# Kernel tuning notes

Hardware: AMD Instinct MI355X
Metric: run time of the kernel (lower is better)

The kernel has to match this reference:

```python
import jax, jax.numpy as jnp
import numpy as np

B, L, H, NH = 32, 512, 256, 4
DH = H // NH
EPS = 1e-12


def setup_inputs() -> dict:
    key = jax.random.key(0)
    ks = jax.random.split(key, 24)
    p = lambda k, shape: 0.02 * jax.random.normal(k, shape, dtype=jnp.float32)
    return {
        "input_tensor": jax.random.normal(ks[0], (B, L, H), dtype=jnp.float32),
        # sorted positive timestamps (seconds-like scale)
        "time_seq": jnp.sort(jax.random.uniform(ks[1], (B, L), dtype=jnp.float32) * 100.0, axis=-1),
        "attention_mask": jnp.zeros((B, 1, L, L), dtype=jnp.float32),
        "item_seq_len": jnp.clip(jax.random.randint(ks[2], (B,), 0, L), 2, L),
        "Wq": p(ks[3], (H, H)), "bq": jnp.zeros((H,), jnp.float32),
        "Wk": p(ks[4], (H, H)), "bk": jnp.zeros((H,), jnp.float32),
        "Wv": p(ks[5], (H, H)), "bv": jnp.zeros((H,), jnp.float32),
        "Wd": p(ks[6], (H, H)), "bd": jnp.zeros((H,), jnp.float32),
        "ln_g": jnp.ones((H,), jnp.float32), "ln_b": jnp.zeros((H,), jnp.float32),
        "Wtq": p(ks[7], (H, H)), "btq": jnp.zeros((H,), jnp.float32),
        "tw1": p(ks[8], (L, L)), "tb1": p(ks[9], (L, L)),
        "tow1": p(ks[10], (L, L)), "tow2": p(ks[11], (L, L)), "tob": p(ks[12], (L, L)),
        "Wt": p(ks[13], (1, 2 * H)), "bt": jnp.zeros((1,), jnp.float32),
    }


def reference(input_tensor, time_seq, attention_mask, item_seq_len,
              Wq, bq, Wk, bk, Wv, bv, Wd, bd, ln_g, ln_b,
              Wtq, btq, tw1, tb1, tow1, tow2, tob, Wt, bt):
    x = input_tensor  # (B, L, H)

    def heads(t):  # (B,L,H) -> (B,NH,L,DH)
        return t.reshape(B, L, NH, DH).transpose(0, 2, 1, 3)

    q = heads(x @ Wq.T + bq)
    k = heads(x @ Wk.T + bk)
    v = heads(x @ Wv.T + bv)

    scores = jnp.einsum('bhqd,bhkd->bhqk', q, k)  # (B,NH,L,L)

    # --- time decay gate ---
    tq = x @ Wtq.T + btq                                  # (B,L,H)
    time_query_key = jnp.tanh(jnp.einsum('bqh,bkh->bqk', tq, x))  # (B,L,L)
    diff = jnp.abs(time_seq[:, :, None] - time_seq[:, None, :])   # |t_i - t_j|
    decay = jnp.tanh(jnp.log1p(diff) * tw1 + tb1)
    decay_gate = tow1 * decay + tow2 * time_query_key + tob       # (B,L,L)
    time_attn = jax.nn.sigmoid(decay_gate)[:, None, :, :]         # (B,1,L,L)

    scores = scores * time_attn / jnp.sqrt(jnp.float32(DH)) + attention_mask
    probs = jax.nn.softmax(scores, axis=-1)

    ctx = jnp.einsum('bhqk,bhkd->bhqd', probs, v)
    ctx = ctx.transpose(0, 2, 1, 3).reshape(B, L, H)

    hs = ctx @ Wd.T + bd + x
    mu = jnp.mean(hs, axis=-1, keepdims=True)
    var = jnp.var(hs, axis=-1, keepdims=True)
    hs = (hs - mu) / jnp.sqrt(var + EPS) * ln_g + ln_b   # (B,L,H)

    bidx = jnp.arange(B)
    emb1 = hs[bidx, item_seq_len - 1]  # (B,H)
    emb2 = hs[bidx, item_seq_len - 2]  # (B,H)
    pred_intervals = jnp.concatenate([emb1, emb2], axis=1) @ Wt.T + bt  # (B,1)
    return hs, pred_intervals
```

## Files before the change

kernel.cpp:

```cpp
#include <hip/hip_runtime.h>
#include <math.h>

#define Bn 32
#define Ln 512
#define Hn 256
#define NHn 4
#define DHn 64

typedef __attribute__((ext_vector_type(8))) short bf16x8;
typedef __attribute__((ext_vector_type(4))) float f32x4;
typedef unsigned int uint32;

__device__ __forceinline__ short f2b(float f) {
    union { float f; uint32 u; } v; v.f = f;
    uint32 r = (v.u + 0x7FFFu + ((v.u >> 16) & 1u)) >> 16;
    return (short)r;
}
__device__ __forceinline__ float b2f(short h) {
    union { uint32 u; float f; } v; v.u = ((uint32)(unsigned short)h) << 16;
    return v.f;
}
__device__ __forceinline__ float fast_tanh(float x) {
    float e = __expf(2.f * x);
    return 1.f - 2.f * __builtin_amdgcn_rcpf(e + 1.f);
}
__device__ __forceinline__ float fast_sigmoid(float x) {
    return __builtin_amdgcn_rcpf(1.f + __expf(-x));
}

__global__ __launch_bounds__(256) void conv_kernel(
    const float* __restrict__ x,
    const float* __restrict__ Wq, const float* __restrict__ Wk,
    const float* __restrict__ Wv, const float* __restrict__ Wtq,
    const float* __restrict__ Wd,
    short* __restrict__ xb, short* __restrict__ wb)
{
    const size_t NLH = (size_t)Bn * Ln * Hn;
    size_t i4 = ((size_t)blockIdx.x * 256 + threadIdx.x) * 4;
    if (i4 < NLH) {
        float4 v = *(const float4*)(x + i4);
        short4 o; o.x = f2b(v.x); o.y = f2b(v.y); o.z = f2b(v.z); o.w = f2b(v.w);
        *(short4*)(xb + i4) = o;
    } else {
        size_t off = i4 - NLH;
        int w = (int)(off >> 16);
        size_t wi = off & 65535;
        const float* src = (w == 0) ? Wq : (w == 1) ? Wk : (w == 2) ? Wv : (w == 3) ? Wtq : Wd;
        float4 v = *(const float4*)(src + wi);
        short4 o; o.x = f2b(v.x); o.y = f2b(v.y); o.z = f2b(v.z); o.w = f2b(v.w);
        *(short4*)(wb + off) = o;
    }
}

struct Acc { f32x4 t[4]; };

__device__ __forceinline__ void gemm_tile_64(
    const short* __restrict__ A,
    const short* __restrict__ Bm,
    int K, short* As, short* Bs, Acc& acc)
{
    const int tid = threadIdx.x;
    const int lane = tid & 63, w = tid >> 6;
    const int quad = lane >> 4, lm = lane & 15;
    const int srow = tid >> 3;
    const int slot = tid & 7;

    for (int k0 = 0; k0 < K; k0 += 64) {
        __syncthreads();
#pragma unroll
        for (int iss = 0; iss < 2; ++iss) {
            int r = srow + iss * 32;
            bf16x8 av = *(const bf16x8*)(A + (size_t)r * K + k0 + slot * 8);
            bf16x8 bv = *(const bf16x8*)(Bm + (size_t)r * K + k0 + slot * 8);
            *(bf16x8*)(As + r * 72 + slot * 8) = av;
            *(bf16x8*)(Bs + r * 72 + slot * 8) = bv;
        }
        __syncthreads();
#pragma unroll
        for (int ks = 0; ks < 2; ++ks) {
            bf16x8 a = *(const bf16x8*)(As + (w * 16 + lm) * 72 + ks * 32 + quad * 8);
#pragma unroll
            for (int kt = 0; kt < 4; ++kt) {
                bf16x8 b = *(const bf16x8*)(Bs + (kt * 16 + lm) * 72 + ks * 32 + quad * 8);
                acc.t[kt] = __builtin_amdgcn_mfma_f32_16x16x32_bf16(a, b, acc.t[kt], 0, 0, 0);
            }
        }
    }
}

__global__ __launch_bounds__(256) void proj_kernel(
    const short* __restrict__ xb, const short* __restrict__ wb,
    const float* __restrict__ bq, const float* __restrict__ bk,
    const float* __restrict__ bv, const float* __restrict__ btq,
    short* __restrict__ qb, short* __restrict__ kb,
    short* __restrict__ vt, short* __restrict__ tqb)
{
    __shared__ short As[64 * 72];
    __shared__ short Bs[64 * 72];
    const int tensor = blockIdx.x >> 2;
    const int ncol0 = (blockIdx.x & 3) * 64;
    const int m0 = blockIdx.y * 64;
    const short* A = xb + (size_t)m0 * Hn;
    const short* Bw = wb + (size_t)tensor * 65536 + (size_t)ncol0 * Hn;
    const float* bias = (tensor == 0) ? bq : (tensor == 1) ? bk : (tensor == 2) ? bv : btq;

    Acc acc;
#pragma unroll
    for (int i = 0; i < 4; ++i) acc.t[i] = (f32x4){0.f, 0.f, 0.f, 0.f};
    gemm_tile_64(A, Bw, Hn, As, Bs, acc);

    const int lane = threadIdx.x & 63, w = threadIdx.x >> 6;
    const int quad = lane >> 4, lm = lane & 15;

    if (tensor == 2) {
#pragma unroll
        for (int kt = 0; kt < 4; ++kt) {
            int n = ncol0 + kt * 16 + lm;
            float bs = bv[n];
            int h = n >> 6, d = n & 63;
#pragma unroll
            for (int r = 0; r < 4; ++r) {
                int row = m0 + w * 16 + quad * 4 + r;
                int bb = row >> 9, l = row & 511;
                vt[((size_t)(bb * NHn + h) * DHn + d) * Ln + l] = f2b(acc.t[kt][r] + bs);
            }
        }
    } else {
        short* out = (tensor == 0) ? qb : (tensor == 1) ? kb : tqb;
#pragma unroll
        for (int kt = 0; kt < 4; ++kt) {
            int n = ncol0 + kt * 16 + lm;
            float bs = bias[n];
#pragma unroll
            for (int r = 0; r < 4; ++r) {
                int row = m0 + w * 16 + quad * 4 + r;
                out[(size_t)row * Hn + n] = f2b(acc.t[kt][r] + bs);
            }
        }
    }
}

__global__ __launch_bounds__(256) void gate_kernel(
    const short* __restrict__ tqb, const short* __restrict__ xb,
    const float* __restrict__ tseq,
    const float* __restrict__ tw1, const float* __restrict__ tb1,
    const float* __restrict__ tow1, const float* __restrict__ tow2,
    const float* __restrict__ tob,
    short* __restrict__ gateb)
{
    __shared__ short As[64 * 72];
    __shared__ short Bs[64 * 72];
    const int b = blockIdx.z;
    const int m0 = blockIdx.y * 64, n0 = blockIdx.x * 64;
    const short* A = tqb + ((size_t)b * Ln + m0) * Hn;
    const short* Bw = xb + ((size_t)b * Ln + n0) * Hn;

    Acc acc;
#pragma unroll
    for (int i = 0; i < 4; ++i) acc.t[i] = (f32x4){0.f, 0.f, 0.f, 0.f};
    gemm_tile_64(A, Bw, Hn, As, Bs, acc);

    const int lane = threadIdx.x & 63, w = threadIdx.x >> 6;
    const int quad = lane >> 4, lm = lane & 15;
    const float* ts = tseq + (size_t)b * Ln;
    short* go = gateb + (size_t)b * Ln * Ln;
    float ti[4];
#pragma unroll
    for (int r = 0; r < 4; ++r) ti[r] = ts[m0 + w * 16 + quad * 4 + r];
#pragma unroll
    for (int kt = 0; kt < 4; ++kt) {
        int j = n0 + kt * 16 + lm;
        float tj = ts[j];
#pragma unroll
        for (int r = 0; r < 4; ++r) {
            int i = m0 + w * 16 + quad * 4 + r;
            size_t ij = (size_t)i * Ln + j;
            float lg = __logf(1.f + fabsf(ti[r] - tj));
            float dec = fast_tanh(lg * tw1[ij] + tb1[ij]);
            float tqk = fast_tanh(acc.t[kt][r]);
            float dg = tow1[ij] * dec + tow2[ij] * tqk + tob[ij];
            float g = 0.125f * fast_sigmoid(dg);
            go[ij] = f2b(g);
        }
    }
}

__global__ __launch_bounds__(256) void flash_mfma(
    const short* __restrict__ qb, const short* __restrict__ kb,
    const short* __restrict__ vt, const short* __restrict__ gateb,
    const float* __restrict__ mask, short* __restrict__ ctxb)
{
    __shared__ short Ks[64 * 72];
    __shared__ short Vt[64 * 72];
    __shared__ short Ps[4 * 16 * 72];
    const int h = blockIdx.x;
    const int q0 = blockIdx.y * 64;
    const int b = blockIdx.z;
    const int tid = threadIdx.x;
    const int w = tid >> 6, lane = tid & 63;
    const int quad = lane >> 4, lm = lane & 15;
    const int srow = tid >> 3, slot = tid & 7;

    bf16x8 qf0, qf1;
    {
        const short* qrow = qb + ((size_t)(b * Ln + q0 + w * 16 + lm)) * Hn + h * DHn;
        qf0 = *(const bf16x8*)(qrow + quad * 8);
        qf1 = *(const bf16x8*)(qrow + 32 + quad * 8);
    }

    f32x4 o[4];
#pragma unroll
    for (int i = 0; i < 4; ++i) o[i] = (f32x4){0.f, 0.f, 0.f, 0.f};
    float m_run[4] = {-INFINITY, -INFINITY, -INFINITY, -INFINITY};
    float l_run[4] = {0.f, 0.f, 0.f, 0.f};
    const short* gr_base = gateb + (size_t)b * Ln * Ln;
    const float* mk_base = mask + (size_t)b * Ln * Ln;
    const int qrow0 = q0 + w * 16 + quad * 4;
    const short* kbase = kb + ((size_t)(b * Ln)) * Hn + h * DHn;
    const short* vbase = vt + (size_t)(b * NHn + h) * DHn * Ln;

    for (int k0 = 0; k0 < Ln; k0 += 64) {
        __syncthreads();
#pragma unroll
        for (int iss = 0; iss < 2; ++iss) {
            int r = srow + iss * 32;
            bf16x8 kv = *(const bf16x8*)(kbase + (size_t)(k0 + r) * Hn + slot * 8);
            bf16x8 vv = *(const bf16x8*)(vbase + (size_t)r * Ln + k0 + slot * 8);
            *(bf16x8*)(Ks + r * 72 + slot * 8) = kv;
            *(bf16x8*)(Vt + r * 72 + slot * 8) = vv;
        }
        __syncthreads();

        f32x4 s[4];
#pragma unroll
        for (int kt = 0; kt < 4; ++kt) {
            s[kt] = (f32x4){0.f, 0.f, 0.f, 0.f};
            bf16x8 b0 = *(const bf16x8*)(Ks + (kt * 16 + lm) * 72 + quad * 8);
            s[kt] = __builtin_amdgcn_mfma_f32_16x16x32_bf16(qf0, b0, s[kt], 0, 0, 0);
            bf16x8 b1 = *(const bf16x8*)(Ks + (kt * 16 + lm) * 72 + 32 + quad * 8);
            s[kt] = __builtin_amdgcn_mfma_f32_16x16x32_bf16(qf1, b1, s[kt], 0, 0, 0);
        }

        float mnew[4];
#pragma unroll
        for (int r = 0; r < 4; ++r) mnew[r] = m_run[r];
#pragma unroll
        for (int kt = 0; kt < 4; ++kt) {
            int col = k0 + kt * 16 + lm;
#pragma unroll
            for (int r = 0; r < 4; ++r) {
                float g  = b2f(gr_base[(size_t)(qrow0 + r) * Ln + col]);
                float mv = mk_base[(size_t)(qrow0 + r) * Ln + col];
                float sv = s[kt][r] * g + mv;
                s[kt][r] = sv;
                mnew[r] = fmaxf(mnew[r], sv);
            }
        }
        float alpha[4], rsum[4];
#pragma unroll
        for (int r = 0; r < 4; ++r) {
#pragma unroll
            for (int off = 1; off < 16; off <<= 1)
                mnew[r] = fmaxf(mnew[r], __shfl_xor(mnew[r], off, 64));
            alpha[r] = __expf(m_run[r] - mnew[r]);
            m_run[r] = mnew[r];
            rsum[r] = 0.f;
        }
        float p[4][4];
#pragma unroll
        for (int kt = 0; kt < 4; ++kt)
#pragma unroll
            for (int r = 0; r < 4; ++r) {
                float pv = __expf(s[kt][r] - m_run[r]);
                p[kt][r] = pv;
                rsum[r] += pv;
            }
#pragma unroll
        for (int r = 0; r < 4; ++r) {
#pragma unroll
            for (int off = 1; off < 16; off <<= 1) rsum[r] += __shfl_xor(rsum[r], off, 64);
            l_run[r] = l_run[r] * alpha[r] + rsum[r];
#pragma unroll
            for (int ot = 0; ot < 4; ++ot) o[ot][r] *= alpha[r];
        }
        short* pw = Ps + w * 16 * 72;
#pragma unroll
        for (int kt = 0; kt < 4; ++kt)
#pragma unroll
            for (int r = 0; r < 4; ++r)
                pw[(quad * 4 + r) * 72 + kt * 16 + lm] = f2b(p[kt][r]);

#pragma unroll
        for (int ks = 0; ks < 2; ++ks) {
            bf16x8 pa = *(const bf16x8*)(pw + lm * 72 + ks * 32 + quad * 8);
#pragma unroll
            for (int ot = 0; ot < 4; ++ot) {
                bf16x8 vv = *(const bf16x8*)(Vt + (ot * 16 + lm) * 72 + ks * 32 + quad * 8);
                o[ot] = __builtin_amdgcn_mfma_f32_16x16x32_bf16(pa, vv, o[ot], 0, 0, 0);
            }
        }
    }

    float inv[4];
#pragma unroll
    for (int r = 0; r < 4; ++r) inv[r] = 1.0f / l_run[r];
#pragma unroll
    for (int ot = 0; ot < 4; ++ot) {
        int d = h * DHn + ot * 16 + lm;
#pragma unroll
        for (int r = 0; r < 4; ++r) {
            int row = b * Ln + qrow0 + r;
            ctxb[(size_t)row * Hn + d] = f2b(o[ot][r] * inv[r]);
        }
    }
}

__global__ __launch_bounds__(256) void outproj_ln_kernel(
    const short* __restrict__ ctxb, const short* __restrict__ wdb,
    const float* __restrict__ bd, const float* __restrict__ x,
    const float* __restrict__ g, const float* __restrict__ beta,
    float* __restrict__ out)
{
    const int m0 = blockIdx.x * 64;
    const int tid = threadIdx.x;
    const int lane = tid & 63, w = tid >> 6;
    const int quad = lane >> 4, lm = lane & 15;

    const short* arow = ctxb + (size_t)(m0 + w * 16 + lm) * Hn;
    bf16x8 af[8];
#pragma unroll
    for (int k8 = 0; k8 < 8; ++k8)
        af[k8] = *(const bf16x8*)(arow + k8 * 32 + quad * 8);

    f32x4 acc[4][4];
#pragma unroll
    for (int i = 0; i < 4; ++i)
#pragma unroll
        for (int j = 0; j < 4; ++j) acc[i][j] = (f32x4){0.f, 0.f, 0.f, 0.f};

#pragma unroll
    for (int k8 = 0; k8 < 8; ++k8) {
#pragma unroll
        for (int nt = 0; nt < 4; ++nt)
#pragma unroll
            for (int kt = 0; kt < 4; ++kt) {
                bf16x8 bf = *(const bf16x8*)(wdb + (size_t)(nt * 64 + kt * 16 + lm) * Hn + k8 * 32 + quad * 8);
                acc[nt][kt] = __builtin_amdgcn_mfma_f32_16x16x32_bf16(af[k8], bf, acc[nt][kt], 0, 0, 0);
            }
    }

    const int rl0 = w * 16 + quad * 4;
    float s1[4] = {0.f, 0.f, 0.f, 0.f}, s2[4] = {0.f, 0.f, 0.f, 0.f};
#pragma unroll
    for (int nt = 0; nt < 4; ++nt)
#pragma unroll
        for (int kt = 0; kt < 4; ++kt) {
            int col = nt * 64 + kt * 16 + lm;
            float bdv = bd[col];
#pragma unroll
            for (int r = 0; r < 4; ++r) {
                float xv = x[(size_t)(m0 + rl0 + r) * Hn + col];
                float hv = acc[nt][kt][r] + bdv + xv;
                acc[nt][kt][r] = hv;
                s1[r] += hv;
                s2[r] += hv * hv;
            }
        }
#pragma unroll
    for (int r = 0; r < 4; ++r) {
#pragma unroll
        for (int off = 1; off < 16; off <<= 1) {
            s1[r] += __shfl_xor(s1[r], off, 64);
            s2[r] += __shfl_xor(s2[r], off, 64);
        }
    }
    float mu[4], rstd[4];
#pragma unroll
    for (int r = 0; r < 4; ++r) {
        mu[r] = s1[r] * (1.f / 256.f);
        float var = s2[r] * (1.f / 256.f) - mu[r] * mu[r];
        rstd[r] = rsqrtf(var + 1e-12f);
    }
#pragma unroll
    for (int nt = 0; nt < 4; ++nt)
#pragma unroll
        for (int kt = 0; kt < 4; ++kt) {
            int col = nt * 64 + kt * 16 + lm;
            float gv = g[col], bb = beta[col];
#pragma unroll
            for (int r = 0; r < 4; ++r)
                out[(size_t)(m0 + rl0 + r) * Hn + col] =
                    (acc[nt][kt][r] - mu[r]) * rstd[r] * gv + bb;
        }
}

__global__ __launch_bounds__(256) void pred_kernel(const float* __restrict__ hs,
                                                   const int* __restrict__ lens,
                                                   const float* __restrict__ Wt,
                                                   const float* __restrict__ bt,
                                                   float* __restrict__ pred)
{
    const int b = blockIdx.x, t = threadIdx.x;
    int len = lens[b];
    float e1 = hs[((size_t)b * Ln + (len - 1)) * Hn + t];
    float e2 = hs[((size_t)b * Ln + (len - 2)) * Hn + t];
    float v = e1 * Wt[t] + e2 * Wt[Hn + t];
#pragma unroll
    for (int off = 32; off > 0; off >>= 1) v += __shfl_xor(v, off, 64);
    __shared__ float ps[4];
    if ((t & 63) == 0) ps[t >> 6] = v;
    __syncthreads();
    if (t == 0) pred[b] = ps[0] + ps[1] + ps[2] + ps[3] + bt[0];
}

extern "C" void kernel_launch(void* const* d_in, const int* in_sizes, int n_in,
                              void* d_out, int out_size, void* d_ws, size_t ws_size,
                              hipStream_t stream) {
    (void)in_sizes; (void)n_in; (void)out_size; (void)ws_size;
    const float* x    = (const float*)d_in[0];
    const float* tseq = (const float*)d_in[1];
    const float* mask = (const float*)d_in[2];
    const int*   lens = (const int*)d_in[3];
    const float* Wq = (const float*)d_in[4];  const float* bq = (const float*)d_in[5];
    const float* Wk = (const float*)d_in[6];  const float* bk = (const float*)d_in[7];
    const float* Wv = (const float*)d_in[8];  const float* bv = (const float*)d_in[9];
    const float* Wd = (const float*)d_in[10]; const float* bd = (const float*)d_in[11];
    const float* ln_g = (const float*)d_in[12]; const float* ln_b = (const float*)d_in[13];
    const float* Wtq = (const float*)d_in[14]; const float* btq = (const float*)d_in[15];
    const float* tw1 = (const float*)d_in[16]; const float* tb1 = (const float*)d_in[17];
    const float* tow1 = (const float*)d_in[18]; const float* tow2 = (const float*)d_in[19];
    const float* tob = (const float*)d_in[20];
    const float* Wt = (const float*)d_in[21]; const float* bt = (const float*)d_in[22];

    const size_t NLH = (size_t)Bn * Ln * Hn;
    short* ws = (short*)d_ws;
    short* xb    = ws;
    short* wb    = xb + NLH;
    short* qb    = wb + 5 * 65536;
    short* kb    = qb + NLH;
    short* vt    = kb + NLH;
    short* tqb   = vt + NLH;
    short* gateb = tqb + NLH;
    short* ctxb  = tqb;
    float* out   = (float*)d_out;

    dim3 blk(256);
    conv_kernel<<<dim3(4416), blk, 0, stream>>>(x, Wq, Wk, Wv, Wtq, Wd, xb, wb);
    proj_kernel<<<dim3(16, 256), blk, 0, stream>>>(xb, wb, bq, bk, bv, btq, qb, kb, vt, tqb);
    gate_kernel<<<dim3(8, 8, Bn), blk, 0, stream>>>(tqb, xb, tseq, tw1, tb1, tow1, tow2, tob, gateb);
    flash_mfma<<<dim3(NHn, 8, Bn), blk, 0, stream>>>(qb, kb, vt, gateb, mask, ctxb);
    outproj_ln_kernel<<<dim3(256), blk, 0, stream>>>(ctxb, wb + 4 * 65536, bd, x, ln_g, ln_b, out);
    pred_kernel<<<dim3(Bn), blk, 0, stream>>>(out, lens, Wt, bt, out + NLH);
}
```

Before: 234.9 us.

## Shrink flash attention blocks to 32 queries and prefetch gate/mask before MFMA

Each flash-attention block now holds two waves covering 32 query rows instead of four waves covering 64, which doubles the grid to 2048 blocks. The grid axes are reordered so the head index moves to y and the query tile to x. Gate and mask values are loaded into registers before the QK^T MFMAs so their global-load latency overlaps the matrix math. In exchange, each K/V tile is reloaded by twice as many blocks, and the extra prefetch registers may lower occupancy.

```diff
diff --git a/kernel.cpp b/kernel.cpp
--- a/kernel.cpp
+++ b/kernel.cpp
@@ -185,21 +185,19 @@
     }
 }
 
-__global__ __launch_bounds__(256) void flash_mfma(
+__global__ __launch_bounds__(128) void flash_mfma(
     const short* __restrict__ qb, const short* __restrict__ kb,
     const short* __restrict__ vt, const short* __restrict__ gateb,
     const float* __restrict__ mask, short* __restrict__ ctxb)
 {
     __shared__ short Ks[64 * 72];
     __shared__ short Vt[64 * 72];
-    __shared__ short Ps[4 * 16 * 72];
-    const int h = blockIdx.x;
-    const int q0 = blockIdx.y * 64;
-    const int b = blockIdx.z;
+    __shared__ short Ps[2 * 16 * 72];
+    const int q0 = blockIdx.x * 32;
+    const int h = blockIdx.y, b = blockIdx.z;
     const int tid = threadIdx.x;
     const int w = tid >> 6, lane = tid & 63;
     const int quad = lane >> 4, lm = lane & 15;
-    const int srow = tid >> 3, slot = tid & 7;
 
     bf16x8 qf0, qf1;
     {
@@ -222,14 +220,26 @@
     for (int k0 = 0; k0 < Ln; k0 += 64) {
         __syncthreads();
 #pragma unroll
-        for (int iss = 0; iss < 2; ++iss) {
-            int r = srow + iss * 32;
-            bf16x8 kv = *(const bf16x8*)(kbase + (size_t)(k0 + r) * Hn + slot * 8);
-            bf16x8 vv = *(const bf16x8*)(vbase + (size_t)r * Ln + k0 + slot * 8);
-            *(bf16x8*)(Ks + r * 72 + slot * 8) = kv;
-            *(bf16x8*)(Vt + r * 72 + slot * 8) = vv;
+        for (int i = 0; i < 4; ++i) {
+            int e = i * 128 + tid;
+            int r = e >> 3, sl = e & 7;
+            bf16x8 kv = *(const bf16x8*)(kbase + (size_t)(k0 + r) * Hn + sl * 8);
+            bf16x8 vv = *(const bf16x8*)(vbase + (size_t)r * Ln + k0 + sl * 8);
+            *(bf16x8*)(Ks + r * 72 + sl * 8) = kv;
+            *(bf16x8*)(Vt + r * 72 + sl * 8) = vv;
         }
         __syncthreads();
+
+        float gvv[4][4], mvv[4][4];
+#pragma unroll
+        for (int kt = 0; kt < 4; ++kt) {
+            int col = k0 + kt * 16 + lm;
+#pragma unroll
+            for (int r = 0; r < 4; ++r) {
+                gvv[kt][r] = b2f(gr_base[(size_t)(qrow0 + r) * Ln + col]);
+                mvv[kt][r] = mk_base[(size_t)(qrow0 + r) * Ln + col];
+            }
+        }
 
         f32x4 s[4];
 #pragma unroll
@@ -245,17 +255,13 @@
 #pragma unroll
         for (int r = 0; r < 4; ++r) mnew[r] = m_run[r];
 #pragma unroll
-        for (int kt = 0; kt < 4; ++kt) {
-            int col = k0 + kt * 16 + lm;
-#pragma unroll
-            for (int r = 0; r < 4; ++r) {
-                float g  = b2f(gr_base[(size_t)(qrow0 + r) * Ln + col]);
-                float mv = mk_base[(size_t)(qrow0 + r) * Ln + col];
-                float sv = s[kt][r] * g + mv;
+        for (int kt = 0; kt < 4; ++kt)
+#pragma unroll
+            for (int r = 0; r < 4; ++r) {
+                float sv = s[kt][r] * gvv[kt][r] + mvv[kt][r];
                 s[kt][r] = sv;
                 mnew[r] = fmaxf(mnew[r], sv);
             }
-        }
         float alpha[4], rsum[4];
 #pragma unroll
         for (int r = 0; r < 4; ++r) {
@@ -448,7 +454,7 @@
     conv_kernel<<<dim3(4416), blk, 0, stream>>>(x, Wq, Wk, Wv, Wtq, Wd, xb, wb);
     proj_kernel<<<dim3(16, 256), blk, 0, stream>>>(xb, wb, bq, bk, bv, btq, qb, kb, vt, tqb);
     gate_kernel<<<dim3(8, 8, Bn), blk, 0, stream>>>(tqb, xb, tseq, tw1, tb1, tow1, tow2, tob, gateb);
-    flash_mfma<<<dim3(NHn, 8, Bn), blk, 0, stream>>>(qb, kb, vt, gateb, mask, ctxb);
+    flash_mfma<<<dim3(16, NHn, Bn), dim3(128), 0, stream>>>(qb, kb, vt, gateb, mask, ctxb);
     outproj_ln_kernel<<<dim3(256), blk, 0, stream>>>(ctxb, wb + 4 * 65536, bd, x, ln_g, ln_b, out);
     pred_kernel<<<dim3(Bn), blk, 0, stream>>>(out, lens, Wt, bt, out + NLH);
 }
```

New measurement: 240.1 us. 1.02x slower.

## Store gate in MFMA fragment layout and remap block order for XCD locality

Applied to the files above, without the earlier changes.

The gate kernel now writes its bf16 gate values in a per-thread tiled layout that matches the flash kernel's MFMA accumulator fragment. The flash kernel can then read each 64x64 tile with two 16-byte vector loads instead of 16 scattered 2-byte loads. The mask loads are hoisted ahead of the QK MFMAs so their latency overlaps compute, and the flash grid is reordered so query blocks of one head are adjacent. The proj kernel also remaps its block index so each XCD works on a contiguous row range, aiming for better L2 reuse. The gate buffer layout is now private to this pair of kernels.

```diff
diff --git a/kernel.cpp b/kernel.cpp
--- a/kernel.cpp
+++ b/kernel.cpp
@@ -97,9 +97,12 @@
 {
     __shared__ short As[64 * 72];
     __shared__ short Bs[64 * 72];
-    const int tensor = blockIdx.x >> 2;
-    const int ncol0 = (blockIdx.x & 3) * 64;
-    const int m0 = blockIdx.y * 64;
+    const int bid = blockIdx.y * 16 + blockIdx.x;
+    const int xcd = bid & 7, idx = bid >> 3;
+    const int v = xcd * 512 + idx;
+    const int tensor = (v & 15) >> 2;
+    const int ncol0 = (v & 3) * 64;
+    const int m0 = (v >> 4) * 64;
     const short* A = xb + (size_t)m0 * Hn;
     const short* Bw = wb + (size_t)tensor * 65536 + (size_t)ncol0 * Hn;
     const float* bias = (tensor == 0) ? bq : (tensor == 1) ? bk : (tensor == 2) ? bv : btq;
@@ -160,13 +163,15 @@
     for (int i = 0; i < 4; ++i) acc.t[i] = (f32x4){0.f, 0.f, 0.f, 0.f};
     gemm_tile_64(A, Bw, Hn, As, Bs, acc);
 
-    const int lane = threadIdx.x & 63, w = threadIdx.x >> 6;
+    const int tid = threadIdx.x;
+    const int lane = tid & 63, w = tid >> 6;
     const int quad = lane >> 4, lm = lane & 15;
     const float* ts = tseq + (size_t)b * Ln;
-    short* go = gateb + (size_t)b * Ln * Ln;
     float ti[4];
 #pragma unroll
     for (int r = 0; r < 4; ++r) ti[r] = ts[m0 + w * 16 + quad * 4 + r];
+
+    bf16x8 g01, g23;
 #pragma unroll
     for (int kt = 0; kt < 4; ++kt) {
         int j = n0 + kt * 16 + lm;
@@ -180,9 +185,13 @@
             float tqk = fast_tanh(acc.t[kt][r]);
             float dg = tow1[ij] * dec + tow2[ij] * tqk + tob[ij];
             float g = 0.125f * fast_sigmoid(dg);
-            go[ij] = f2b(g);
-        }
-    }
+            if (kt < 2) g01[kt * 4 + r] = f2b(g);
+            else        g23[(kt - 2) * 4 + r] = f2b(g);
+        }
+    }
+    size_t base = ((((size_t)b * 8 + blockIdx.y) * 8 + blockIdx.x) * 256 + tid) * 16;
+    *(bf16x8*)(gateb + base) = g01;
+    *(bf16x8*)(gateb + base + 8) = g23;
 }
 
 __global__ __launch_bounds__(256) void flash_mfma(
@@ -193,9 +202,9 @@
     __shared__ short Ks[64 * 72];
     __shared__ short Vt[64 * 72];
     __shared__ short Ps[4 * 16 * 72];
-    const int h = blockIdx.x;
-    const int q0 = blockIdx.y * 64;
-    const int b = blockIdx.z;
+    const int mb = blockIdx.x;
+    const int q0 = mb * 64;
+    const int h = blockIdx.y, b = blockIdx.z;
     const int tid = threadIdx.x;
     const int w = tid >> 6, lane = tid & 63;
     const int quad = lane >> 4, lm = lane & 15;
@@ -213,11 +222,11 @@
     for (int i = 0; i < 4; ++i) o[i] = (f32x4){0.f, 0.f, 0.f, 0.f};
     float m_run[4] = {-INFINITY, -INFINITY, -INFINITY, -INFINITY};
     float l_run[4] = {0.f, 0.f, 0.f, 0.f};
-    const short* gr_base = gateb + (size_t)b * Ln * Ln;
     const float* mk_base = mask + (size_t)b * Ln * Ln;
     const int qrow0 = q0 + w * 16 + quad * 4;
     const short* kbase = kb + ((size_t)(b * Ln)) * Hn + h * DHn;
     const short* vbase = vt + (size_t)(b * NHn + h) * DHn * Ln;
+    const short* gtile0 = gateb + (((size_t)b * 8 + mb) * 8 * 256 + tid) * 16;
 
     for (int k0 = 0; k0 < Ln; k0 += 64) {
         __syncthreads();
@@ -231,6 +240,18 @@
         }
         __syncthreads();
 
+        const short* gt = gtile0 + (size_t)(k0 >> 6) * 256 * 16;
+        bf16x8 g01 = *(const bf16x8*)(gt);
+        bf16x8 g23 = *(const bf16x8*)(gt + 8);
+        float mvv[4][4];
+#pragma unroll
+        for (int kt = 0; kt < 4; ++kt) {
+            int col = k0 + kt * 16 + lm;
+#pragma unroll
+            for (int r = 0; r < 4; ++r)
+                mvv[kt][r] = mk_base[(size_t)(qrow0 + r) * Ln + col];
+        }
+
         f32x4 s[4];
 #pragma unroll
         for (int kt = 0; kt < 4; ++kt) {
@@ -245,17 +266,14 @@
 #pragma unroll
         for (int r = 0; r < 4; ++r) mnew[r] = m_run[r];
 #pragma unroll
-        for (int kt = 0; kt < 4; ++kt) {
-            int col = k0 + kt * 16 + lm;
+        for (int kt = 0; kt < 4; ++kt)
 #pragma unroll
             for (int r = 0; r < 4; ++r) {
-                float g  = b2f(gr_base[(size_t)(qrow0 + r) * Ln + col]);
-                float mv = mk_base[(size_t)(qrow0 + r) * Ln + col];
-                float sv = s[kt][r] * g + mv;
+                float g = b2f(kt < 2 ? g01[(kt & 1) * 4 + r] : g23[(kt & 1) * 4 + r]);
+                float sv = s[kt][r] * g + mvv[kt][r];
                 s[kt][r] = sv;
                 mnew[r] = fmaxf(mnew[r], sv);
             }
-        }
         float alpha[4], rsum[4];
 #pragma unroll
         for (int r = 0; r < 4; ++r) {
@@ -448,7 +466,7 @@
     conv_kernel<<<dim3(4416), blk, 0, stream>>>(x, Wq, Wk, Wv, Wtq, Wd, xb, wb);
     proj_kernel<<<dim3(16, 256), blk, 0, stream>>>(xb, wb, bq, bk, bv, btq, qb, kb, vt, tqb);
     gate_kernel<<<dim3(8, 8, Bn), blk, 0, stream>>>(tqb, xb, tseq, tw1, tb1, tow1, tow2, tob, gateb);
-    flash_mfma<<<dim3(NHn, 8, Bn), blk, 0, stream>>>(qb, kb, vt, gateb, mask, ctxb);
+    flash_mfma<<<dim3(8, NHn, Bn), blk, 0, stream>>>(qb, kb, vt, gateb, mask, ctxb);
     outproj_ln_kernel<<<dim3(256), blk, 0, stream>>>(ctxb, wb + 4 * 65536, bd, x, ln_g, ln_b, out);
     pred_kernel<<<dim3(Bn), blk, 0, stream>>>(out, lens, Wt, bt, out + NLH);
 }
```

After: 232.9 us. About the same (-0.9%).
